# Kernel optimization log

Hardware: AMD Instinct MI355X
Metric: run time of the kernel (lower is better)

The kernel has to match this reference:

```python
import jax, jax.numpy as jnp
import numpy as np

B, T, E, H = 4, 2048, 2048, 16
HD = E // H  # 128


def apply_rope(x, freqs):
    # x: (B, T, H, HD); freqs: (T, HD//2) rotation angles per position/pair
    cos = jnp.cos(freqs)[None, :, None, :]  # (1, T, 1, HD//2)
    sin = jnp.sin(freqs)[None, :, None, :]
    xr = x.reshape(*x.shape[:-1], HD // 2, 2)
    x1, x2 = xr[..., 0], xr[..., 1]
    out = jnp.stack([x1 * cos - x2 * sin, x1 * sin + x2 * cos], axis=-1)
    return out.reshape(x.shape)


def setup_inputs() -> dict:
    key = jax.random.key(0)
    k1, k2, k3, k4 = jax.random.split(key, 4)
    x = jax.random.normal(k1, (B, T, E), dtype=jnp.float32)
    freqs = jax.random.uniform(k2, (T, HD // 2), dtype=jnp.float32) * 6.28318
    w_qkv = jax.random.normal(k3, (3 * E, E), dtype=jnp.float32) * 0.02
    w_o = jax.random.normal(k4, (E, E), dtype=jnp.float32) * 0.02
    return {"x": x, "freqs": freqs, "w_qkv": w_qkv, "w_o": w_o}


def reference(x, freqs, w_qkv, w_o):
    b, t, e = x.shape
    qkv = x @ w_qkv.T                            # (B, T, 3E)
    qkv = qkv.reshape(b, t, 3, H, HD)
    q, k, v = qkv[:, :, 0], qkv[:, :, 1], qkv[:, :, 2]
    q = apply_rope(q, freqs)
    k = apply_rope(k, freqs)
    q = q.transpose(0, 2, 1, 3)                  # (B, H, T, HD)
    k = k.transpose(0, 2, 1, 3)
    v = v.transpose(0, 2, 1, 3)
    scale = 1.0 / np.sqrt(HD)
    scores = jnp.einsum('bhqd,bhkd->bhqk', q, k) * scale
    causal = jnp.tril(jnp.ones((t, t), dtype=bool))
    scores = jnp.where(causal[None, None], scores, jnp.finfo(scores.dtype).min)
    attn = jax.nn.softmax(scores, axis=-1)
    out = jnp.einsum('bhqk,bhkd->bhqd', attn, v)  # (B, H, T, HD)
    out = out.transpose(0, 2, 1, 3).reshape(b, t, e)
    return out @ w_o.T
```

## Files before the change

kernel.cpp:

```cpp
#include <hip/hip_runtime.h>
#include <type_traits>

#define DEV __device__ __forceinline__

typedef __attribute__((ext_vector_type(4))) float f32x4;
typedef __attribute__((ext_vector_type(8))) __bf16 bf16x8;
typedef __attribute__((ext_vector_type(8))) short s16x8;
typedef unsigned int u32;
typedef unsigned short u16;

DEV u16 f2bf(float f) {
  u32 u = __builtin_bit_cast(u32, f);
  u32 r = u + 0x7FFFu + ((u >> 16) & 1u);
  return (u16)(r >> 16);
}
DEV float bf2f(u16 h) {
  u32 u = ((u32)h) << 16;
  return __builtin_bit_cast(float, u);
}

template <typename A>
DEV auto mfma_sel(A a, A b, f32x4 c, int)
    -> decltype(__builtin_amdgcn_mfma_f32_16x16x32_bf16(a, b, c, 0, 0, 0)) {
  return __builtin_amdgcn_mfma_f32_16x16x32_bf16(a, b, c, 0, 0, 0);
}
template <typename A>
DEV f32x4 mfma_sel(A a, A b, f32x4 c, long) {
  using O = typename std::conditional<std::is_same<A, bf16x8>::value, s16x8, bf16x8>::type;
  return __builtin_amdgcn_mfma_f32_16x16x32_bf16(
      __builtin_bit_cast(O, a), __builtin_bit_cast(O, b), c, 0, 0, 0);
}
DEV f32x4 MFMA16(bf16x8 a, bf16x8 b, f32x4 c) { return mfma_sel(a, b, c, 0); }

DEV void gload_lds16(const void* g, void* l) {
  __builtin_amdgcn_global_load_lds(
      (__attribute__((address_space(1))) void*)(g),
      (__attribute__((address_space(3))) void*)(l), 16, 0, 0);
}

__global__ __launch_bounds__(256) void cvt_f32_bf16(const float* __restrict__ in,
                                                    u16* __restrict__ out, int n4) {
  int i = blockIdx.x * blockDim.x + threadIdx.x;
  const int stride = gridDim.x * blockDim.x;
  for (; i < n4; i += stride) {
    const float4 v = ((const float4*)in)[i];
    ushort4 o;
    o.x = f2bf(v.x); o.y = f2bf(v.y); o.z = f2bf(v.z); o.w = f2bf(v.w);
    ((ushort4*)out)[i] = o;
  }
}

__global__ __launch_bounds__(256) void build_cst(const float* __restrict__ freqs,
                                                 float2* __restrict__ cst, int n) {
  int i = blockIdx.x * blockDim.x + threadIdx.x;
  if (i < n) {
    float f = freqs[i];
    cst[i] = make_float2(cosf(f), sinf(f));
  }
}

template <int MODE>
__global__ __launch_bounds__(512, 2) void gemm_bt(const u16* __restrict__ A,
                                                  const u16* __restrict__ Bm,
                                                  void* __restrict__ Cp,
                                                  u16* __restrict__ q_r,
                                                  u16* __restrict__ k_r,
                                                  u16* __restrict__ v_r,
                                                  const float2* __restrict__ cst,
                                                  const int M, const int N, const int K) {
  __shared__ __align__(16) u16 As[4][256 * 32];
  __shared__ __align__(16) u16 Bs[4][256 * 32];
  const int tid = threadIdx.x;
  const int wid = tid >> 6;
  const int lane = tid & 63;
  const int lrow = lane & 15;
  const int lgrp = lane >> 4;

  const int gx = gridDim.x;
  const int nwg = gx * gridDim.y;
  int id = blockIdx.y * gx + blockIdx.x;
  const int cpx = nwg >> 3;
  id = (id & 7) * cpx + (id >> 3);
  const int row0 = (id / gx) * 256;
  const int col0 = (id % gx) * 256;

  const int wm = (wid >> 2) * 128;
  const int wn = (wid & 3) * 64;

  f32x4 acc[8][4] = {};

  const int sj0 = wid * 2;
  const int srow = lane >> 2;
  const int sc = lane & 3;

#define STAGE_HALF(SLOT, T, II)                                                   \
  do {                                                                            \
    const int j_ = sj0 + (II);                                                    \
    const int row_ = j_ * 16 + srow;                                              \
    const int ch_ = sc ^ ((row_ >> 1) & 3);                                       \
    const int k0_ = (T) * 32;                                                     \
    gload_lds16(A + (size_t)(row0 + row_) * K + k0_ + ch_ * 8,                    \
                (char*)&As[SLOT][0] + j_ * 1024);                                 \
    gload_lds16(Bm + (size_t)(col0 + row_) * K + k0_ + ch_ * 8,                   \
                (char*)&Bs[SLOT][0] + j_ * 1024);                                 \
  } while (0)

#define READS_B(SLOT)                                                             \
  _Pragma("unroll") for (int fn = 0; fn < 4; ++fn) {                              \
    const int brow_ = wn + fn * 16 + lrow;                                        \
    bfr[fn] = *(const bf16x8*)((const char*)&Bs[SLOT][0] + brow_ * 64 +           \
                               ((lgrp ^ ((brow_ >> 1) & 3)) << 4));               \
  }

#define READS_A(SLOT, QUAD)                                                       \
  _Pragma("unroll") for (int i_ = 0; i_ < 4; ++i_) {                              \
    const int arow_ = wm + ((QUAD) * 4 + i_) * 16 + lrow;                         \
    af[i_] = *(const bf16x8*)((const char*)&As[SLOT][0] + arow_ * 64 +            \
                              ((lgrp ^ ((arow_ >> 1) & 3)) << 4));                \
  }

#define MFMA_QUAD(QUAD)                                                           \
  __builtin_amdgcn_s_setprio(1);                                                  \
  _Pragma("unroll") for (int fm = 0; fm < 4; ++fm) {                              \
    _Pragma("unroll") for (int fn = 0; fn < 4; ++fn)                              \
      acc[(QUAD) * 4 + fm][fn] = MFMA16(af[fm], bfr[fn], acc[(QUAD) * 4 + fm][fn]); \
  }                                                                               \
  __builtin_amdgcn_s_setprio(0);

  const int nk = K >> 5;
  STAGE_HALF(0, 0, 0); STAGE_HALF(0, 0, 1);
  STAGE_HALF(1, 1, 0); STAGE_HALF(1, 1, 1);
  STAGE_HALF(2, 2, 0); STAGE_HALF(2, 2, 1);
  __builtin_amdgcn_sched_barrier(0);
  asm volatile("s_waitcnt vmcnt(8)" ::: "memory");
  __builtin_amdgcn_s_barrier();

  bf16x8 bfr[4], af[4];
  for (int t = 0; t < nk - 2; ++t) {
    const int slot = t & 3;
    const int ns = (t + 3) & 3;
    const bool dostage = (t + 3) < nk;
    READS_B(slot)
    READS_A(slot, 0)
    if (dostage) STAGE_HALF(ns, t + 3, 0);
    __builtin_amdgcn_sched_barrier(0);
    __builtin_amdgcn_s_barrier();
    MFMA_QUAD(0)
    __builtin_amdgcn_sched_barrier(0);
    __builtin_amdgcn_s_barrier();
    READS_A(slot, 1)
    if (dostage) STAGE_HALF(ns, t + 3, 1);
    __builtin_amdgcn_sched_barrier(0);
    __builtin_amdgcn_s_barrier();
    MFMA_QUAD(1)
    __builtin_amdgcn_sched_barrier(0);
    asm volatile("s_waitcnt vmcnt(8)" ::: "memory");
    __builtin_amdgcn_s_barrier();
  }
  {
    const int slot = (nk - 2) & 3;
    READS_B(slot) READS_A(slot, 0)
    __builtin_amdgcn_sched_barrier(0);
    __builtin_amdgcn_s_barrier();
    MFMA_QUAD(0)
    __builtin_amdgcn_s_barrier();
    READS_A(slot, 1)
    __builtin_amdgcn_sched_barrier(0);
    __builtin_amdgcn_s_barrier();
    MFMA_QUAD(1)
    __builtin_amdgcn_sched_barrier(0);
    asm volatile("s_waitcnt vmcnt(0)" ::: "memory");
    __builtin_amdgcn_s_barrier();
  }
  {
    const int slot = (nk - 1) & 3;
    READS_B(slot) READS_A(slot, 0)
    __builtin_amdgcn_sched_barrier(0);
    __builtin_amdgcn_s_barrier();
    MFMA_QUAD(0)
    __builtin_amdgcn_s_barrier();
    READS_A(slot, 1)
    MFMA_QUAD(1)
  }

  if constexpr (MODE == 0) {
    #pragma unroll
    for (int fm = 0; fm < 8; ++fm) {
      #pragma unroll
      for (int r = 0; r < 4; ++r) {
        const size_t rb = (size_t)(row0 + wm + fm * 16 + lgrp * 4 + r) * N + col0 + wn + lrow;
        #pragma unroll
        for (int fn = 0; fn < 4; ++fn)
          ((float*)Cp)[rb + fn * 16] = acc[fm][fn][r];
      }
    }
  } else {
    const int which = col0 >> 11;
    const int colw = (col0 & 2047) + wn;
    const int h = colw >> 7;
    const int d0 = colw & 127;
    u16* const dst0 = (which == 0) ? q_r : (which == 1) ? k_r : v_r;
    const bool isv = (which == 2);
    const float wscale = (which == 0) ? (0.08838834765f * 1.44269504089f) : 1.0f;
    #pragma unroll
    for (int fm = 0; fm < 8; ++fm) {
      #pragma unroll
      for (int r = 0; r < 4; ++r) {
        const int grow = row0 + wm + fm * 16 + lgrp * 4 + r;
        const int bb = grow >> 11, tt = grow & 2047;
        u16* const drow = dst0 + (((size_t)(bb * 16 + h) * 2048 + tt) << 7);
        if (isv) {
          #pragma unroll
          for (int fn = 0; fn < 4; ++fn)
            drow[d0 + fn * 16 + lrow] = f2bf(acc[fm][fn][r]);
        } else {
          #pragma unroll
          for (int fn = 0; fn < 4; ++fn) {
            const float v = acc[fm][fn][r];
            const float p = __shfl_xor(v, 1);
            const int d = d0 + fn * 16 + lrow;
            const float2 cs = cst[tt * 64 + (d >> 1)];
            const float o = ((lrow & 1) ? (p * cs.y + v * cs.x) : (v * cs.x - p * cs.y)) * wscale;
            drow[d] = f2bf(o);
          }
        }
      }
    }
  }
#undef STAGE_HALF
#undef READS_B
#undef READS_A
#undef MFMA_QUAD
}

__global__ __launch_bounds__(256) void vtrans(const u16* __restrict__ vr,
                                              u16* __restrict__ vt) {
  constexpr int T = 2048;
  __shared__ u16 tile[64][130];
  const int t0 = blockIdx.x * 64;
  const int bh = blockIdx.y;
  const int tid = threadIdx.x;
  {
    const int tl = tid >> 2;
    const int cg = (tid & 3) * 32;
    const u16* src = vr + ((size_t)bh * T + t0 + tl) * 128 + cg;
    #pragma unroll
    for (int jj = 0; jj < 32; ++jj)
      tile[tl][cg + jj] = src[jj];
  }
  __syncthreads();
  {
    const int d = tid >> 1, half = tid & 1;
    u16* dst = vt + ((size_t)bh * 128 + d) * T + t0 + half * 32;
    #pragma unroll
    for (int jj = 0; jj < 32; ++jj)
      dst[jj] = tile[half * 32 + jj][d];
  }
}

__global__ __launch_bounds__(512, 2) void attn_fwd(const u16* __restrict__ Qp,
                                                   const u16* __restrict__ Kp,
                                                   const u16* __restrict__ Vp,
                                                   u16* __restrict__ Op) {
  constexpr int T = 2048;
  __shared__ __align__(16) u16 Kl[3][64 * 128];
  __shared__ __align__(16) u16 Vl[3][128 * 64];
  __shared__ __align__(16) u16 Pl[8 * 2048];

  const int tid = threadIdx.x;
  const int wid = tid >> 6;
  const int lane = tid & 63;
  const int lrow = lane & 15;
  const int lgrp = lane >> 4;

  const int lin = blockIdx.y * 4 + blockIdx.x;
  const int qa = lin >> 6;
  const int bh = ((lin & 7) << 3) | ((lin >> 3) & 7);

  const u16* Qb = Qp + (size_t)bh * T * 128;
  const u16* Kb = Kp + (size_t)bh * T * 128;
  const u16* Vb = Vp + (size_t)bh * 128 * T;

  const float DTH = 12.0f;
  const int s0 = (lane & 48) + ((lane & 48) >> 2);
  char* Pw = (char*)Pl + wid * 4096;
  const int ob = bh >> 4, oh = bh & 15;

  auto stage = [&](int buf, int kv0) {
    #pragma unroll
    for (int ii = 0; ii < 2; ++ii) {
      const int i = wid * 2 + ii;
      {
        const int rr = i * 4 + (lane >> 4);
        const int cs = (lane & 15) ^ (rr & 7);
        gload_lds16(Kb + (size_t)(kv0 + rr) * 128 + cs * 8, (char*)&Kl[buf][0] + i * 1024);
      }
      {
        const int rr = i * 8 + (lane >> 3);
        const int cs = (lane & 7) ^ (rr & 7);
        gload_lds16(Vb + (size_t)rr * T + kv0 + cs * 8, (char*)&Vl[buf][0] + i * 1024);
      }
    }
  };

  auto process = [&](const int qi) {
    const int q0 = qi * 256;
    const int wq0 = q0 + wid * 32;

    bf16x8 qf[2][4];
    #pragma unroll
    for (int qg = 0; qg < 2; ++qg) {
      const int qrow = wq0 + qg * 16 + lrow;
      #pragma unroll
      for (int db = 0; db < 4; ++db)
        qf[qg][db] = *(const bf16x8*)(Qb + (size_t)qrow * 128 + db * 32 + lgrp * 8);
    }

    f32x4 o[2][8] = {};
    float m[2] = {-3e38f, -3e38f};
    float l[2] = {0.f, 0.f};

    const int nkv = 4 * qi + 4;
    stage(0, 0);
    stage(1, 64);
    int csl = 0;
    for (int j = 0; j < nkv; ++j) {
      if (j < nkv - 1) asm volatile("s_waitcnt vmcnt(4)" ::: "memory");
      else             asm volatile("s_waitcnt vmcnt(0)" ::: "memory");
      __builtin_amdgcn_s_barrier();
      if (j + 2 < nkv) {
        int ss = csl + 2; if (ss >= 3) ss -= 3;
        stage(ss, (j + 2) * 64);
      }
      const int kv0 = j * 64;

      if (kv0 <= wq0 + 31) {
        f32x4 s[2][4] = {};
        __builtin_amdgcn_s_setprio(1);
        #pragma unroll
        for (int t4 = 0; t4 < 4; ++t4) {
          const int krow = t4 * 16 + lrow;
          #pragma unroll
          for (int db = 0; db < 4; ++db) {
            const int ch = (db * 4 + lgrp) ^ (krow & 7);
            bf16x8 kf = *(const bf16x8*)((const char*)&Kl[csl][0] + krow * 256 + ch * 16);
            s[0][t4] = MFMA16(kf, qf[0][db], s[0][t4]);
            s[1][t4] = MFMA16(kf, qf[1][db], s[1][t4]);
          }
        }
        __builtin_amdgcn_s_setprio(0);

        if (kv0 + 63 > wq0) {
          #pragma unroll
          for (int qg = 0; qg < 2; ++qg) {
            const int lim = wq0 + qg * 16 + lrow - kv0 - lgrp * 4;
            #pragma unroll
            for (int t4 = 0; t4 < 4; ++t4) {
              #pragma unroll
              for (int r = 0; r < 4; ++r)
                if (t4 * 16 + r > lim) s[qg][t4][r] = -3e38f;
            }
          }
        }

        float pmax[2];
        #pragma unroll
        for (int qg = 0; qg < 2; ++qg) {
          float pm = fmaxf(fmaxf(s[qg][0][0], s[qg][0][1]), fmaxf(s[qg][0][2], s[qg][0][3]));
          #pragma unroll
          for (int t4 = 1; t4 < 4; ++t4)
            pm = fmaxf(pm, fmaxf(fmaxf(s[qg][t4][0], s[qg][t4][1]),
                                 fmaxf(s[qg][t4][2], s[qg][t4][3])));
          pm = fmaxf(pm, __shfl_xor(pm, 16));
          pm = fmaxf(pm, __shfl_xor(pm, 32));
          pmax[qg] = pm;
        }

        float alpha[2] = {1.f, 1.f};
        const float dmax = fmaxf(pmax[0] - m[0], pmax[1] - m[1]);
        if (__any(dmax > DTH)) {
          #pragma unroll
          for (int qg = 0; qg < 2; ++qg) {
            const float mn = fmaxf(m[qg], pmax[qg]);
            alpha[qg] = exp2f(m[qg] - mn);
            m[qg] = mn;
          }
          #pragma unroll
          for (int qg = 0; qg < 2; ++qg) {
            #pragma unroll
            for (int r = 0; r < 4; ++r) {
              const float a4 = __shfl(alpha[qg], s0 + r);
              #pragma unroll
              for (int db = 0; db < 8; ++db)
                o[qg][db][r] *= a4;
            }
          }
        }

        float psum[2] = {0.f, 0.f};
        #pragma unroll
        for (int qg = 0; qg < 2; ++qg) {
          #pragma unroll
          for (int t4 = 0; t4 < 4; ++t4) {
            #pragma unroll
            for (int r = 0; r < 4; ++r) {
              const float p = exp2f(s[qg][t4][r] - m[qg]);
              s[qg][t4][r] = p;
              psum[qg] += p;
            }
          }
          psum[qg] += __shfl_xor(psum[qg], 16);
          psum[qg] += __shfl_xor(psum[qg], 32);
          l[qg] = l[qg] * alpha[qg] + psum[qg];
        }

        #pragma unroll
        for (int qg = 0; qg < 2; ++qg) {
          #pragma unroll
          for (int t4 = 0; t4 < 4; ++t4) {
            uint2 w;
            w.x = (u32)f2bf(s[qg][t4][0]) | ((u32)f2bf(s[qg][t4][1]) << 16);
            w.y = (u32)f2bf(s[qg][t4][2]) | ((u32)f2bf(s[qg][t4][3]) << 16);
            const int off = lrow * 128 + (((t4 * 2 + (lgrp >> 1)) ^ (lrow & 7)) << 4) + (lgrp & 1) * 8;
            *(uint2*)(Pw + qg * 2048 + off) = w;
          }
        }
        asm volatile("s_waitcnt lgkmcnt(0)" ::: "memory");
        __builtin_amdgcn_sched_barrier(0);

        bf16x8 pa[2][2];
        #pragma unroll
        for (int qg = 0; qg < 2; ++qg) {
          #pragma unroll
          for (int kb = 0; kb < 2; ++kb)
            pa[qg][kb] = *(const bf16x8*)(Pw + qg * 2048 + lrow * 128 +
                                          (((kb * 4 + lgrp) ^ (lrow & 7)) << 4));
        }
        __builtin_amdgcn_s_setprio(1);
        #pragma unroll
        for (int db = 0; db < 8; ++db) {
          const int vrow = db * 16 + lrow;
          #pragma unroll
          for (int kb = 0; kb < 2; ++kb) {
            const int vch = (kb * 4 + lgrp) ^ (vrow & 7);
            bf16x8 vf = *(const bf16x8*)((const char*)&Vl[csl][0] + vrow * 128 + vch * 16);
            o[0][db] = MFMA16(pa[0][kb], vf, o[0][db]);
            o[1][db] = MFMA16(pa[1][kb], vf, o[1][db]);
          }
        }
        __builtin_amdgcn_s_setprio(0);
      }
      csl = (csl == 2) ? 0 : csl + 1;
    }

    #pragma unroll
    for (int qg = 0; qg < 2; ++qg) {
      const float inv = 1.f / l[qg];
      float inv4[4];
      #pragma unroll
      for (int r = 0; r < 4; ++r) inv4[r] = __shfl(inv, s0 + r);
      #pragma unroll
      for (int db = 0; db < 8; ++db) {
        #pragma unroll
        for (int r = 0; r < 4; ++r) {
          const int qrow = wq0 + qg * 16 + lgrp * 4 + r;
          Op[((size_t)ob * T + qrow) * 2048 + oh * 128 + db * 16 + lrow] =
              f2bf(o[qg][db][r] * inv4[r]);
        }
      }
    }
  };

  process(7 - qa);
  __syncthreads();
  process(qa);
}

extern "C" void kernel_launch(void* const* d_in, const int* in_sizes, int n_in,
                              void* d_out, int out_size, void* d_ws, size_t ws_size,
                              hipStream_t stream) {
  const float* x = (const float*)d_in[0];
  const float* freqs = (const float*)d_in[1];
  const float* w_qkv = (const float*)d_in[2];
  const float* w_o = (const float*)d_in[3];

  constexpr int B = 4, T = 2048, E = 2048, H = 16;
  constexpr size_t M = (size_t)B * T;
  constexpr int N3 = 3 * E;

  char* ws = (char*)d_ws;
  size_t off = 0;
  auto alloc = [&](size_t bytes) {
    void* p = ws + off;
    off += (bytes + 255) & ~(size_t)255;
    return p;
  };
  u16* wqkv_bf = (u16*)alloc((size_t)N3 * E * 2);
  u16* wo_bf   = (u16*)alloc((size_t)E * E * 2);
  u16* x_bf    = (u16*)alloc(M * E * 2);
  u16* q_r     = (u16*)alloc(M * E * 2);
  u16* k_r     = (u16*)alloc(M * E * 2);
  u16* v_r     = (u16*)alloc(M * E * 2);
  u16* vt      = (u16*)alloc(M * E * 2);
  u16* attn_o  = (u16*)alloc(M * E * 2);
  float2* cst  = (float2*)alloc((size_t)T * 64 * 8);

  cvt_f32_bf16<<<2048, 256, 0, stream>>>(x, x_bf, (int)(M * E / 4));
  cvt_f32_bf16<<<2048, 256, 0, stream>>>(w_qkv, wqkv_bf, N3 * E / 4);
  cvt_f32_bf16<<<2048, 256, 0, stream>>>(w_o, wo_bf, E * E / 4);
  build_cst<<<(T * 64) / 256, 256, 0, stream>>>(freqs, cst, T * 64);

  gemm_bt<2><<<dim3(N3 / 256, (int)(M / 256)), 512, 0, stream>>>(
      x_bf, wqkv_bf, nullptr, q_r, k_r, v_r, cst, (int)M, N3, E);
  vtrans<<<dim3(T / 64, B * H), 256, 0, stream>>>(v_r, vt);
  attn_fwd<<<dim3(4, B * H), 512, 0, stream>>>(q_r, k_r, vt, attn_o);
  gemm_bt<0><<<dim3(E / 256, (int)(M / 256)), 512, 0, stream>>>(
      attn_o, wo_bf, d_out, nullptr, nullptr, nullptr, nullptr, (int)M, E, E);
}
```

Baseline: 463.5 us.

## Restructure GEMM main loop with register double-buffering and one barrier per k-step

The bf16 MFMA GEMM main loop is rewritten so each k-step waits once on the global-to-LDS copies and passes one workgroup barrier instead of four. The next tile's B and first-half A fragments are prefetched from LDS into a second register set, ping-ponged across a two-step unrolled loop. Both halves of the next stage are issued together, and the separate tail iterations are folded into the loop. The goal is less barrier and sync overhead and more overlap of LDS reads with MFMA work. The cost is higher register pressure and a loop that assumes an even number of k-steps.

```diff
diff --git a/kernel.cpp b/kernel.cpp
--- a/kernel.cpp
+++ b/kernel.cpp
@@ -105,82 +105,58 @@
                 (char*)&Bs[SLOT][0] + j_ * 1024);                                 \
   } while (0)
 
-#define READS_B(SLOT)                                                             \
+#define READS_B_TO(DST, SLOT)                                                     \
   _Pragma("unroll") for (int fn = 0; fn < 4; ++fn) {                              \
     const int brow_ = wn + fn * 16 + lrow;                                        \
-    bfr[fn] = *(const bf16x8*)((const char*)&Bs[SLOT][0] + brow_ * 64 +           \
+    DST[fn] = *(const bf16x8*)((const char*)&Bs[SLOT][0] + brow_ * 64 +           \
                                ((lgrp ^ ((brow_ >> 1) & 3)) << 4));               \
   }
 
-#define READS_A(SLOT, QUAD)                                                       \
+#define READS_A_TO(DST, SLOT, QUAD)                                               \
   _Pragma("unroll") for (int i_ = 0; i_ < 4; ++i_) {                              \
     const int arow_ = wm + ((QUAD) * 4 + i_) * 16 + lrow;                         \
-    af[i_] = *(const bf16x8*)((const char*)&As[SLOT][0] + arow_ * 64 +            \
-                              ((lgrp ^ ((arow_ >> 1) & 3)) << 4));                \
-  }
-
-#define MFMA_QUAD(QUAD)                                                           \
+    DST[i_] = *(const bf16x8*)((const char*)&As[SLOT][0] + arow_ * 64 +           \
+                               ((lgrp ^ ((arow_ >> 1) & 3)) << 4));               \
+  }
+
+#define MFMA_Q(QUAD, AARR, BARR)                                                  \
   __builtin_amdgcn_s_setprio(1);                                                  \
   _Pragma("unroll") for (int fm = 0; fm < 4; ++fm) {                              \
     _Pragma("unroll") for (int fn = 0; fn < 4; ++fn)                              \
-      acc[(QUAD) * 4 + fm][fn] = MFMA16(af[fm], bfr[fn], acc[(QUAD) * 4 + fm][fn]); \
+      acc[(QUAD) * 4 + fm][fn] = MFMA16(AARR[fm], BARR[fn], acc[(QUAD) * 4 + fm][fn]); \
   }                                                                               \
   __builtin_amdgcn_s_setprio(0);
+
+#define BODY(T, BCUR, ACUR, BNXT, ANXT)                                           \
+  do {                                                                            \
+    const int t_ = (T);                                                           \
+    const int slot_ = t_ & 3;                                                     \
+    if (t_ <= nk - 3) asm volatile("s_waitcnt vmcnt(4)" ::: "memory");            \
+    else              asm volatile("s_waitcnt vmcnt(0)" ::: "memory");            \
+    __builtin_amdgcn_s_barrier();                                                 \
+    if (t_ + 3 < nk) { STAGE_HALF((t_ + 3) & 3, t_ + 3, 0);                       \
+                       STAGE_HALF((t_ + 3) & 3, t_ + 3, 1); }                     \
+    if (t_ + 1 < nk) { READS_B_TO(BNXT, (t_ + 1) & 3)                             \
+                       READS_A_TO(ANXT, (t_ + 1) & 3, 0) }                        \
+    READS_A_TO(a1, slot_, 1)                                                      \
+    MFMA_Q(0, ACUR, BCUR)                                                         \
+    MFMA_Q(1, a1, BCUR)                                                           \
+  } while (0)
 
   const int nk = K >> 5;
   STAGE_HALF(0, 0, 0); STAGE_HALF(0, 0, 1);
   STAGE_HALF(1, 1, 0); STAGE_HALF(1, 1, 1);
   STAGE_HALF(2, 2, 0); STAGE_HALF(2, 2, 1);
-  __builtin_amdgcn_sched_barrier(0);
   asm volatile("s_waitcnt vmcnt(8)" ::: "memory");
   __builtin_amdgcn_s_barrier();
 
-  bf16x8 bfr[4], af[4];
-  for (int t = 0; t < nk - 2; ++t) {
-    const int slot = t & 3;
-    const int ns = (t + 3) & 3;
-    const bool dostage = (t + 3) < nk;
-    READS_B(slot)
-    READS_A(slot, 0)
-    if (dostage) STAGE_HALF(ns, t + 3, 0);
-    __builtin_amdgcn_sched_barrier(0);
-    __builtin_amdgcn_s_barrier();
-    MFMA_QUAD(0)
-    __builtin_amdgcn_sched_barrier(0);
-    __builtin_amdgcn_s_barrier();
-    READS_A(slot, 1)
-    if (dostage) STAGE_HALF(ns, t + 3, 1);
-    __builtin_amdgcn_sched_barrier(0);
-    __builtin_amdgcn_s_barrier();
-    MFMA_QUAD(1)
-    __builtin_amdgcn_sched_barrier(0);
-    asm volatile("s_waitcnt vmcnt(8)" ::: "memory");
-    __builtin_amdgcn_s_barrier();
-  }
-  {
-    const int slot = (nk - 2) & 3;
-    READS_B(slot) READS_A(slot, 0)
-    __builtin_amdgcn_sched_barrier(0);
-    __builtin_amdgcn_s_barrier();
-    MFMA_QUAD(0)
-    __builtin_amdgcn_s_barrier();
-    READS_A(slot, 1)
-    __builtin_amdgcn_sched_barrier(0);
-    __builtin_amdgcn_s_barrier();
-    MFMA_QUAD(1)
-    __builtin_amdgcn_sched_barrier(0);
-    asm volatile("s_waitcnt vmcnt(0)" ::: "memory");
-    __builtin_amdgcn_s_barrier();
-  }
-  {
-    const int slot = (nk - 1) & 3;
-    READS_B(slot) READS_A(slot, 0)
-    __builtin_amdgcn_sched_barrier(0);
-    __builtin_amdgcn_s_barrier();
-    MFMA_QUAD(0)
-    __builtin_amdgcn_s_barrier();
-    READS_A(slot, 1)
-    MFMA_QUAD(1)
+  bf16x8 bA[4], aA[4], bB[4], aB[4], a1[4];
+  READS_B_TO(bA, 0)
+  READS_A_TO(aA, 0, 0)
+
+  for (int t = 0; t < nk; t += 2) {
+    BODY(t,     bA, aA, bB, aB);
+    BODY(t + 1, bB, aB, bA, aA);
   }
 
   if constexpr (MODE == 0) {
@@ -228,9 +204,10 @@
     }
   }
 #undef STAGE_HALF
-#undef READS_B
-#undef READS_A
-#undef MFMA_QUAD
+#undef READS_B_TO
+#undef READS_A_TO
+#undef MFMA_Q
+#undef BODY
 }
 
 __global__ __launch_bounds__(256) void vtrans(const u16* __restrict__ vr,
```

After: 524.5 us. 13.1% more time.

## Fuse V transpose into QKV GEMM epilogue via shared-memory staging

Applied to the files above, without the earlier changes.

Removes the separate vtrans kernel and the intermediate v_r buffer. The V-column blocks of the QKV GEMM stage their accumulator tile in shared memory, unified into a single buffer, and write V directly in transposed (B,H,D,T) layout with 16-byte stores. This saves one kernel launch and a full write plus read of the V tensor. In exchange the V blocks get extra barriers and LDS traffic in the epilogue, with a 260-element row stride to limit bank conflicts.

```diff
diff --git a/kernel.cpp b/kernel.cpp
--- a/kernel.cpp
+++ b/kernel.cpp
@@ -65,11 +65,10 @@
                                                   void* __restrict__ Cp,
                                                   u16* __restrict__ q_r,
                                                   u16* __restrict__ k_r,
-                                                  u16* __restrict__ v_r,
+                                                  u16* __restrict__ v_t,
                                                   const float2* __restrict__ cst,
                                                   const int M, const int N, const int K) {
-  __shared__ __align__(16) u16 As[4][256 * 32];
-  __shared__ __align__(16) u16 Bs[4][256 * 32];
+  __shared__ __align__(16) u16 SH[65536];
   const int tid = threadIdx.x;
   const int wid = tid >> 6;
   const int lane = tid & 63;
@@ -100,23 +99,23 @@
     const int ch_ = sc ^ ((row_ >> 1) & 3);                                       \
     const int k0_ = (T) * 32;                                                     \
     gload_lds16(A + (size_t)(row0 + row_) * K + k0_ + ch_ * 8,                    \
-                (char*)&As[SLOT][0] + j_ * 1024);                                 \
+                (char*)SH + (SLOT) * 16384 + j_ * 1024);                          \
     gload_lds16(Bm + (size_t)(col0 + row_) * K + k0_ + ch_ * 8,                   \
-                (char*)&Bs[SLOT][0] + j_ * 1024);                                 \
+                (char*)SH + 65536 + (SLOT) * 16384 + j_ * 1024);                  \
   } while (0)
 
 #define READS_B(SLOT)                                                             \
   _Pragma("unroll") for (int fn = 0; fn < 4; ++fn) {                              \
     const int brow_ = wn + fn * 16 + lrow;                                        \
-    bfr[fn] = *(const bf16x8*)((const char*)&Bs[SLOT][0] + brow_ * 64 +           \
-                               ((lgrp ^ ((brow_ >> 1) & 3)) << 4));               \
+    bfr[fn] = *(const bf16x8*)((const char*)SH + 65536 + (SLOT) * 16384 +         \
+                               brow_ * 64 + ((lgrp ^ ((brow_ >> 1) & 3)) << 4));  \
   }
 
 #define READS_A(SLOT, QUAD)                                                       \
   _Pragma("unroll") for (int i_ = 0; i_ < 4; ++i_) {                              \
     const int arow_ = wm + ((QUAD) * 4 + i_) * 16 + lrow;                         \
-    af[i_] = *(const bf16x8*)((const char*)&As[SLOT][0] + arow_ * 64 +            \
-                              ((lgrp ^ ((arow_ >> 1) & 3)) << 4));                \
+    af[i_] = *(const bf16x8*)((const char*)SH + (SLOT) * 16384 +                  \
+                              arow_ * 64 + ((lgrp ^ ((arow_ >> 1) & 3)) << 4));   \
   }
 
 #define MFMA_QUAD(QUAD)                                                           \
@@ -196,24 +195,19 @@
     }
   } else {
     const int which = col0 >> 11;
-    const int colw = (col0 & 2047) + wn;
-    const int h = colw >> 7;
-    const int d0 = colw & 127;
-    u16* const dst0 = (which == 0) ? q_r : (which == 1) ? k_r : v_r;
-    const bool isv = (which == 2);
-    const float wscale = (which == 0) ? (0.08838834765f * 1.44269504089f) : 1.0f;
-    #pragma unroll
-    for (int fm = 0; fm < 8; ++fm) {
+    if (which < 2) {
+      const int colw = (col0 & 2047) + wn;
+      const int h = colw >> 7;
+      const int d0 = colw & 127;
+      u16* const dst0 = (which == 0) ? q_r : k_r;
+      const float wscale = (which == 0) ? (0.08838834765f * 1.44269504089f) : 1.0f;
       #pragma unroll
-      for (int r = 0; r < 4; ++r) {
-        const int grow = row0 + wm + fm * 16 + lgrp * 4 + r;
-        const int bb = grow >> 11, tt = grow & 2047;
-        u16* const drow = dst0 + (((size_t)(bb * 16 + h) * 2048 + tt) << 7);
-        if (isv) {
-          #pragma unroll
-          for (int fn = 0; fn < 4; ++fn)
-            drow[d0 + fn * 16 + lrow] = f2bf(acc[fm][fn][r]);
-        } else {
+      for (int fm = 0; fm < 8; ++fm) {
+        #pragma unroll
+        for (int r = 0; r < 4; ++r) {
+          const int grow = row0 + wm + fm * 16 + lgrp * 4 + r;
+          const int bb = grow >> 11, tt = grow & 2047;
+          u16* const drow = dst0 + (((size_t)(bb * 16 + h) * 2048 + tt) << 7);
           #pragma unroll
           for (int fn = 0; fn < 4; ++fn) {
             const float v = acc[fm][fn][r];
@@ -225,37 +219,47 @@
           }
         }
       }
+    } else {
+      const int hbase = (col0 - 4096) >> 7;
+      const int bb = row0 >> 11;
+      const int tloc0 = row0 & 2047;
+      const int hd = tid >> 1, half = tid & 1;
+      const int hh = hd >> 7, dd = hd & 127;
+      u16* const dstb = v_t + ((size_t)(bb * 16 + hbase + hh) * 128 + dd) * 2048;
+      #pragma unroll
+      for (int c = 0; c < 2; ++c) {
+        __builtin_amdgcn_s_barrier();
+        if ((wm >> 7) == c) {
+          #pragma unroll
+          for (int fm = 0; fm < 8; ++fm) {
+            #pragma unroll
+            for (int r = 0; r < 4; ++r) {
+              const int rl = fm * 16 + lgrp * 4 + r;
+              #pragma unroll
+              for (int fn = 0; fn < 4; ++fn)
+                SH[rl * 260 + wn + fn * 16 + lrow] = f2bf(acc[fm][fn][r]);
+            }
+          }
+        }
+        __builtin_amdgcn_s_barrier();
+        u16* dst = dstb + tloc0 + c * 128 + half * 64;
+        #pragma unroll
+        for (int seg = 0; seg < 8; ++seg) {
+          const int tb = (half * 64 + seg * 8) * 260 + hd;
+          u32 w0 = (u32)SH[tb]        | ((u32)SH[tb + 260] << 16);
+          u32 w1 = (u32)SH[tb + 520]  | ((u32)SH[tb + 780] << 16);
+          u32 w2 = (u32)SH[tb + 1040] | ((u32)SH[tb + 1300] << 16);
+          u32 w3 = (u32)SH[tb + 1560] | ((u32)SH[tb + 1820] << 16);
+          uint4 w = make_uint4(w0, w1, w2, w3);
+          *(uint4*)(dst + seg * 8) = w;
+        }
+      }
     }
   }
 #undef STAGE_HALF
 #undef READS_B
 #undef READS_A
 #undef MFMA_QUAD
-}
-
-__global__ __launch_bounds__(256) void vtrans(const u16* __restrict__ vr,
-                                              u16* __restrict__ vt) {
-  constexpr int T = 2048;
-  __shared__ u16 tile[64][130];
-  const int t0 = blockIdx.x * 64;
-  const int bh = blockIdx.y;
-  const int tid = threadIdx.x;
-  {
-    const int tl = tid >> 2;
-    const int cg = (tid & 3) * 32;
-    const u16* src = vr + ((size_t)bh * T + t0 + tl) * 128 + cg;
-    #pragma unroll
-    for (int jj = 0; jj < 32; ++jj)
-      tile[tl][cg + jj] = src[jj];
-  }
-  __syncthreads();
-  {
-    const int d = tid >> 1, half = tid & 1;
-    u16* dst = vt + ((size_t)bh * 128 + d) * T + t0 + half * 32;
-    #pragma unroll
-    for (int jj = 0; jj < 32; ++jj)
-      dst[jj] = tile[half * 32 + jj][d];
-  }
 }
 
 __global__ __launch_bounds__(512, 2) void attn_fwd(const u16* __restrict__ Qp,
@@ -500,7 +504,6 @@
   u16* x_bf    = (u16*)alloc(M * E * 2);
   u16* q_r     = (u16*)alloc(M * E * 2);
   u16* k_r     = (u16*)alloc(M * E * 2);
-  u16* v_r     = (u16*)alloc(M * E * 2);
   u16* vt      = (u16*)alloc(M * E * 2);
   u16* attn_o  = (u16*)alloc(M * E * 2);
   float2* cst  = (float2*)alloc((size_t)T * 64 * 8);
@@ -511,8 +514,7 @@
   build_cst<<<(T * 64) / 256, 256, 0, stream>>>(freqs, cst, T * 64);
 
   gemm_bt<2><<<dim3(N3 / 256, (int)(M / 256)), 512, 0, stream>>>(
-      x_bf, wqkv_bf, nullptr, q_r, k_r, v_r, cst, (int)M, N3, E);
-  vtrans<<<dim3(T / 64, B * H), 256, 0, stream>>>(v_r, vt);
+      x_bf, wqkv_bf, nullptr, q_r, k_r, vt, cst, (int)M, N3, E);
   attn_fwd<<<dim3(4, B * H), 512, 0, stream>>>(q_r, k_r, vt, attn_o);
   gemm_bt<0><<<dim3(E / 256, (int)(M / 256)), 512, 0, stream>>>(
       attn_o, wo_bf, d_out, nullptr, nullptr, nullptr, nullptr, (int)M, E, E);
```

After: 437.0 us. 5.7% less time.
